# Kernel tuning notes

Hardware: AMD Instinct MI355X
Metric: run time of the kernel (lower is better)

The kernel has to match this reference:

```python
import jax, jax.numpy as jnp
import numpy as np

NUM_SPHERICAL = 7   # L
NUM_RADIAL = 6      # K
CUTOFF = 5.0
ENV_P = 6           # envelope exponent 5 -> p = exponent + 1
N_EDGES = 500000
N_PAIRS = 2000000


def _sph_jn_np(r, l):
    # spherical Bessel j_l via upward recurrence (numpy float64, host-side)
    j = np.sin(r) / r
    if l == 0:
        return j
    jp = np.sin(r) / r**2 - np.cos(r) / r
    for i in range(1, l):
        j, jp = jp, (2 * i + 1) / r * jp - j
    return jp


def _bessel_zeros(L, K):
    # zeros of j_0 are n*pi; zeros of j_l interlace zeros of j_{l-1} (bisection)
    prev = np.arange(1, K + L + 1, dtype=np.float64) * np.pi
    zeros = [prev[:K].copy()]
    for l in range(1, L):
        lo, hi = prev[:-1].copy(), prev[1:].copy()
        flo = _sph_jn_np(lo, l)
        for _ in range(100):
            mid = 0.5 * (lo + hi)
            fm = _sph_jn_np(mid, l)
            same = np.sign(fm) == np.sign(flo)
            lo = np.where(same, mid, lo)
            flo = np.where(same, fm, flo)
            hi = np.where(same, hi, mid)
        prev = 0.5 * (lo + hi)
        zeros.append(prev[:K].copy())
    return np.stack(zeros)  # (L, K)


_Z = _bessel_zeros(NUM_SPHERICAL, NUM_RADIAL)
_NORM = np.stack([1.0 / np.sqrt(0.5 * _sph_jn_np(_Z[l], l + 1) ** 2)
                  for l in range(NUM_SPHERICAL)])
Z = jnp.asarray(_Z, dtype=jnp.float32)        # (L, K) Bessel zeros z_{l,n}
NORM = jnp.asarray(_NORM, dtype=jnp.float32)  # (L, K) normalizers c_{l,n}
_SPH_C = jnp.asarray(np.sqrt((2 * np.arange(NUM_SPHERICAL) + 1) / (4 * np.pi)),
                     dtype=jnp.float32)       # Y_l^0 prefactors


def _sph_jn(t, l):
    # spherical Bessel j_l(t), upward recurrence (matches closed-form sympy basis)
    j = jnp.sin(t) / t
    if l == 0:
        return j
    jp = jnp.sin(t) / t**2 - jnp.cos(t) / t
    for i in range(1, l):
        j, jp = jp, (2 * i + 1) / t * jp - j
    return jp


def _envelope(x):
    # DimeNet polynomial envelope u(x) = 1/x + a x^{p-1} + b x^p + c x^{p+1}
    p = ENV_P
    a = -(p + 1) * (p + 2) / 2.0
    b = float(p * (p + 2))
    c = -p * (p + 1) / 2.0
    return 1.0 / x + a * x ** (p - 1) + b * x ** p + c * x ** (p + 1)


def setup_inputs() -> dict:
    key = jax.random.key(0)
    k1, k2, k3 = jax.random.split(key, 3)
    distances = jax.random.normal(k1, (N_EDGES, 3), dtype=jnp.float32) * 2.0
    senders = jax.random.randint(k2, (N_PAIRS,), 0, N_EDGES)
    receivers = jax.random.randint(k3, (N_PAIRS,), 0, N_EDGES)
    return {"distances": distances, "senders": senders, "receivers": receivers}


def reference(distances, senders, receivers):
    L, K = NUM_SPHERICAL, NUM_RADIAL
    dist = jnp.linalg.norm(distances, axis=-1, keepdims=True)     # (E, 1)
    normed_d = distances / dist                                   # (E, 3)
    x = dist / CUTOFF                                             # (E, 1)
    # radial Bessel basis: rbf[e, l, n] = c_{l,n} * j_l(z_{l,n} * x_e)
    rbf = jnp.stack([NORM[l] * _sph_jn(x * Z[l], l) for l in range(L)], axis=1)
    env = _envelope(x)                                            # (E, 1)
    rbf = rbf.reshape(-1, L * K) * env                            # (E, L*K)
    # angular basis: Y_l^0(theta) = sqrt((2l+1)/4pi) * P_l(cos theta)
    cos = jnp.einsum('pd,pd->p', normed_d[receivers], normed_d[senders])  # (P,)
    P_prev = jnp.ones_like(cos)
    P_cur = cos
    legs = [P_prev, P_cur]
    for l in range(1, L - 1):
        P_prev, P_cur = P_cur, ((2 * l + 1) * cos * P_cur - l * P_prev) / (l + 1)
        legs.append(P_cur)
    cbf = jnp.stack(legs[:L], axis=1) * _SPH_C                    # (P, L)
    # outer-product fuse: (P, L, K) -> (P, L*K)
    out = (rbf[senders].reshape(-1, L, K) * cbf[:, :, None]).reshape(-1, L * K)
    return out
```

## Files before the change

### kernel.cpp

```cpp
#include <hip/hip_runtime.h>
#include <math.h>

#define L_SPH 7
#define K_RAD 6
#define LK    42
#define TPB   256
#define PTPB  64
#define RSTR  48


typedef float f32x4 __attribute__((ext_vector_type(4)));
typedef float f32x2 __attribute__((ext_vector_type(2)));


struct SBConsts {
    float z[L_SPH][K_RAD];
    float nrm[L_SPH][K_RAD];
    float sphc[L_SPH];
};

static double host_sph_jn(double r, int l) {
    double j = sin(r) / r;
    if (l == 0) return j;
    double jp = sin(r) / (r * r) - cos(r) / r;
    for (int i = 1; i < l; i++) {
        double t = (2.0 * i + 1.0) / r * jp - j;
        j = jp; jp = t;
    }
    return jp;
}

static SBConsts make_consts() {
    const int L = L_SPH, K = K_RAD;
    double prev[L + K];
    for (int i = 0; i < L + K; i++) prev[i] = (i + 1) * M_PI;
    int plen = L + K;
    double zeros[L_SPH][K_RAD];
    for (int n = 0; n < K; n++) zeros[0][n] = prev[n];
    for (int l = 1; l < L; l++) {
        int m = plen - 1;
        double lo[L + K], hi[L + K], flo[L + K];
        for (int i = 0; i < m; i++) {
            lo[i] = prev[i]; hi[i] = prev[i + 1];
            flo[i] = host_sph_jn(lo[i], l);
        }
        for (int it = 0; it < 100; it++) {
            for (int i = 0; i < m; i++) {
                double mid = 0.5 * (lo[i] + hi[i]);
                double fm  = host_sph_jn(mid, l);
                bool same  = (fm >= 0.0) == (flo[i] >= 0.0);
                if (same) { lo[i] = mid; flo[i] = fm; }
                else      { hi[i] = mid; }
            }
        }
        for (int i = 0; i < m; i++) prev[i] = 0.5 * (lo[i] + hi[i]);
        plen = m;
        for (int n = 0; n < K; n++) zeros[l][n] = prev[n];
    }
    SBConsts c;
    for (int l = 0; l < L; l++) {
        for (int n = 0; n < K; n++) {
            c.z[l][n] = (float)zeros[l][n];
            double j1 = host_sph_jn(zeros[l][n], l + 1);
            c.nrm[l][n] = (float)(1.0 / sqrt(0.5 * j1 * j1));
        }
        c.sphc[l] = (float)sqrt((2.0 * l + 1.0) / (4.0 * M_PI));
    }
    return c;
}


__device__ __forceinline__ float sin_f32cr(float t) { return (float)sin((double)t); }
__device__ __forceinline__ void sincos_f32cr(float t, float& s, float& c) {
    double ds, dc;
    sincos((double)t, &ds, &dc);
    s = (float)ds; c = (float)dc;
}

__device__ void edge_row_f32(float dx, float dy, float dz, const SBConsts& c,
                             float* row, float& nx, float& ny, float& nz) {
#pragma clang fp contract(off)
    float s = dx * dx;
    s = s + dy * dy;
    s = s + dz * dz;
    float dist = (float)sqrt((double)s);
    nx = dx / dist; ny = dy / dist; nz = dz / dist;
    float x = dist / 5.0f;
    float x2 = x * x, x4 = x2 * x2;
    float x5 = x4 * x, x6 = x5 * x, x7 = x6 * x;
    float env = 1.0f / x;
    env = env + (-28.0f) * x5;
    env = env + 48.0f * x6;
    env = env + (-21.0f) * x7;
#pragma unroll
    for (int l = 0; l < L_SPH; l++) {
#pragma unroll
        for (int n = 0; n < K_RAD; n++) {
            float t  = x * c.z[l][n];
            float sn, co;
            if (l == 0) { sn = sin_f32cr(t); co = 0.0f; }
            else        { sincos_f32cr(t, sn, co); }
            float j  = sn / t;
            if (l > 0) {
                float t2 = t * t;
                float a1 = sn / t2;
                float a2 = co / t;
                float jp = a1 - a2;
#pragma unroll
                for (int i = 1; i < l; i++) {
                    float q  = (float)(2 * i + 1) / t;
                    float m  = q * jp;
                    float nj = m - j;
                    j = jp; jp = nj;
                }
                j = jp;
            }
            float rb = c.nrm[l][n] * j;
            row[l * K_RAD + n] = rb * env;
        }
    }
}

__device__ __forceinline__ void legendre_cbf(float cs, const float* sphc,
                                             float* cbf) {
#pragma clang fp contract(off)
    float P0 = 1.0f, P1 = cs;
    cbf[0] = sphc[0];
    cbf[1] = sphc[1] * cs;
#pragma unroll
    for (int l = 1; l < L_SPH - 1; l++) {
        float a  = (float)(2 * l + 1) * cs;
        float b  = a * P1;
        float d  = b - (float)l * P0;
        float Pn = d / (float)(l + 1);
        P0 = P1; P1 = Pn;
        cbf[l + 1] = sphc[l + 1] * Pn;
    }
}


__global__ __launch_bounds__(TPB) void edge_kernel(
        const float* __restrict__ d, float* __restrict__ rbf,
        float4* __restrict__ nd4, int nE, SBConsts c) {
    int e = blockIdx.x * TPB + threadIdx.x;
    if (e >= nE) return;
    float dx = d[3 * e], dy = d[3 * e + 1], dz = d[3 * e + 2];
    float row[LK], nx, ny, nz;
    edge_row_f32(dx, dy, dz, c, row, nx, ny, nz);
    nd4[e] = make_float4(nx, ny, nz, 0.0f);
    float4* o = (float4*)(rbf + (size_t)e * RSTR);
#pragma unroll
    for (int q = 0; q < 10; q++)
        o[q] = make_float4(row[4 * q], row[4 * q + 1], row[4 * q + 2], row[4 * q + 3]);
    o[10] = make_float4(row[40], row[41], nx, ny);
    o[11] = make_float4(nz, 0.0f, 0.0f, 0.0f);
}


__global__ __launch_bounds__(PTPB, 4) void pair_kernel(
        const int* __restrict__ snd, const int* __restrict__ rcv,
        const float* __restrict__ rbf, const float4* __restrict__ nd4,
        float* __restrict__ out, int nP, SBConsts c) {
#pragma clang fp contract(off)
    __shared__ float so[PTPB * LK];
    int p = blockIdx.x * PTPB + threadIdx.x;
    if (p < nP) {
        int s = snd[p], r = rcv[p];
        const float4* rowp = (const float4*)(rbf + (size_t)s * RSTR);
        float4 v[12];
#pragma unroll
        for (int q = 0; q < 12; q++) v[q] = rowp[q];
        float4 b = nd4[r];
        float ax = v[10].z, ay = v[10].w, az = v[11].x;
        float cs = ax * b.x;
        cs = cs + ay * b.y;
        cs = cs + az * b.z;
        float cbf[L_SPH];
        legendre_cbf(cs, c.sphc, cbf);
        float2* my = (float2*)&so[threadIdx.x * LK];
#pragma unroll
        for (int q = 0; q < 10; q++) {
            float4 vq = v[q];
            my[2 * q]     = make_float2(vq.x * cbf[(4 * q + 0) / K_RAD],
                                        vq.y * cbf[(4 * q + 1) / K_RAD]);
            my[2 * q + 1] = make_float2(vq.z * cbf[(4 * q + 2) / K_RAD],
                                        vq.w * cbf[(4 * q + 3) / K_RAD]);
        }
        my[20] = make_float2(v[10].x * cbf[6], v[10].y * cbf[6]);
    }
    __syncthreads();
    size_t base  = (size_t)blockIdx.x * (PTPB * LK);
    size_t limit = (size_t)nP * LK;
    if (base + PTPB * LK <= limit) {
        f32x4* o4 = (f32x4*)(out + base);
        const f32x4* s4 = (const f32x4*)so;
#pragma unroll
        for (int k = 0; k < 10; k++)
            __builtin_nontemporal_store(s4[threadIdx.x + k * PTPB],
                                        &o4[threadIdx.x + k * PTPB]);
        f32x2* o2 = (f32x2*)(out + base + 2560);
        const f32x2* s2 = (const f32x2*)(so + 2560);
        __builtin_nontemporal_store(s2[threadIdx.x], &o2[threadIdx.x]);
    } else {
        for (int k = 0; k < LK; k++) {
            size_t g = base + threadIdx.x + (size_t)k * PTPB;
            if (g < limit) out[g] = so[threadIdx.x + k * PTPB];
        }
    }
}


__global__ __launch_bounds__(TPB) void fused_kernel(
        const float* __restrict__ d, const int* __restrict__ snd,
        const int* __restrict__ rcv, float* __restrict__ out,
        int nP, SBConsts c) {
#pragma clang fp contract(off)
    int p = blockIdx.x * TPB + threadIdx.x;
    if (p >= nP) return;
    int s = snd[p], r = rcv[p];
    float row[LK], sx, sy, sz;
    edge_row_f32(d[3 * s], d[3 * s + 1], d[3 * s + 2], c, row, sx, sy, sz);
    float rx = d[3 * r], ry = d[3 * r + 1], rz = d[3 * r + 2];
    float t = rx * rx;  t = t + ry * ry;  t = t + rz * rz;
    float rd = (float)sqrt((double)t);
    float cs = sx * (rx / rd);
    cs = cs + sy * (ry / rd);
    cs = cs + sz * (rz / rd);
    float cbf[L_SPH];
    legendre_cbf(cs, c.sphc, cbf);
    float* o = out + (size_t)p * LK;
#pragma unroll
    for (int j = 0; j < LK; j++) o[j] = row[j] * cbf[j / K_RAD];
}


extern "C" void kernel_launch(void* const* d_in, const int* in_sizes, int n_in,
                              void* d_out, int out_size, void* d_ws, size_t ws_size,
                              hipStream_t stream) {
    static SBConsts c = make_consts();
    const float* dists = (const float*)d_in[0];
    const int*   snd   = (const int*)d_in[1];
    const int*   rcv   = (const int*)d_in[2];
    float*       out   = (float*)d_out;
    int nE = in_sizes[0] / 3;
    int nP = in_sizes[1];

    size_t rbf_bytes = (size_t)nE * RSTR * sizeof(float);
    size_t need = rbf_bytes + (size_t)nE * sizeof(float4);

    if (ws_size >= need) {
        float*  rbf = (float*)d_ws;
        float4* nd4 = (float4*)((char*)d_ws + rbf_bytes);
        edge_kernel<<<(nE + TPB - 1) / TPB, TPB, 0, stream>>>(dists, rbf, nd4, nE, c);
        pair_kernel<<<(nP + PTPB - 1) / PTPB, PTPB, 0, stream>>>(snd, rcv, rbf, nd4, out, nP, c);
    } else {
        fused_kernel<<<(nP + TPB - 1) / TPB, TPB, 0, stream>>>(dists, snd, rcv, out, nP, c);
    }
}
```

Baseline: 586.4 us.

## Split edge basis computation into per-element threads across edges and basis indices

New measurement: 591.0 us. About the same (+0.8%).

```diff
diff --git a/kernel.cpp b/kernel.cpp
--- a/kernel.cpp
+++ b/kernel.cpp
@@ -69,13 +69,159 @@
     return c;
 }
 
-
 __device__ __forceinline__ float sin_f32cr(float t) { return (float)sin((double)t); }
 __device__ __forceinline__ void sincos_f32cr(float t, float& s, float& c) {
     double ds, dc;
     sincos((double)t, &ds, &dc);
     s = (float)ds; c = (float)dc;
 }
+
+__device__ __forceinline__ void legendre_cbf(float cs, const float* sphc,
+                                             float* cbf) {
+#pragma clang fp contract(off)
+    float P0 = 1.0f, P1 = cs;
+    cbf[0] = sphc[0];
+    cbf[1] = sphc[1] * cs;
+#pragma unroll
+    for (int l = 1; l < L_SPH - 1; l++) {
+        float a  = (float)(2 * l + 1) * cs;
+        float b  = a * P1;
+        float d  = b - (float)l * P0;
+        float Pn = d / (float)(l + 1);
+        P0 = P1; P1 = Pn;
+        cbf[l + 1] = sphc[l + 1] * Pn;
+    }
+}
+
+
+__global__ __launch_bounds__(64) void init_tab(float* __restrict__ tab, SBConsts c) {
+    if (blockIdx.x != 0 || threadIdx.x != 0) return;
+#pragma unroll
+    for (int l = 0; l < L_SPH; l++)
+#pragma unroll
+        for (int n = 0; n < K_RAD; n++) {
+            tab[l * K_RAD + n]      = c.z[l][n];
+            tab[42 + l * K_RAD + n] = c.nrm[l][n];
+        }
+}
+
+
+__global__ __launch_bounds__(TPB) void edge_pre(
+        const float* __restrict__ d, float* __restrict__ rbf,
+        float4* __restrict__ nd4, int nE) {
+#pragma clang fp contract(off)
+    int e = blockIdx.x * TPB + threadIdx.x;
+    if (e >= nE) return;
+    float dx = d[3 * e], dy = d[3 * e + 1], dz = d[3 * e + 2];
+    float s = dx * dx;
+    s = s + dy * dy;
+    s = s + dz * dz;
+    float dist = (float)sqrt((double)s);
+    float nx = dx / dist, ny = dy / dist, nz = dz / dist;
+    float x = dist / 5.0f;
+    float x2 = x * x, x4 = x2 * x2;
+    float x5 = x4 * x, x6 = x5 * x, x7 = x6 * x;
+    float env = 1.0f / x;
+    env = env + (-28.0f) * x5;
+    env = env + 48.0f * x6;
+    env = env + (-21.0f) * x7;
+    nd4[e] = make_float4(nx, ny, nz, 0.0f);
+    float* row = rbf + (size_t)e * RSTR;
+    f32x2 xe; xe.x = x; xe.y = env;
+    *(f32x2*)(row + 42) = xe;
+    f32x4 dir; dir.x = nx; dir.y = ny; dir.z = nz; dir.w = 0.0f;
+    *(f32x4*)(row + 44) = dir;
+}
+
+
+__global__ __launch_bounds__(TPB, 4) void edge_basis(
+        const float* __restrict__ tab, float* __restrict__ rbf, int nE) {
+#pragma clang fp contract(off)
+    int i = blockIdx.x * TPB + threadIdx.x;
+    if (i >= nE * LK) return;
+    unsigned ui = (unsigned)i;
+    unsigned e = ui / (unsigned)LK;
+    int j = (int)(ui - e * (unsigned)LK);
+    const float* row = rbf + (size_t)e * RSTR;
+    f32x2 xe = *(const f32x2*)(row + 42);
+    float x = xe.x, env = xe.y;
+    float zj = tab[j], nrmj = tab[42 + j];
+    int l = j / K_RAD;
+    float t = x * zj;
+    float sn, co;
+    if (l == 0) { sn = sin_f32cr(t); co = 0.0f; }
+    else        { sincos_f32cr(t, sn, co); }
+    float jj = sn / t;
+    if (l > 0) {
+        float t2 = t * t;
+        float a1 = sn / t2;
+        float a2 = co / t;
+        float jp = a1 - a2;
+        for (int ii = 1; ii < l; ii++) {
+            float q  = (float)(2 * ii + 1) / t;
+            float m  = q * jp;
+            float nj = m - jj;
+            jj = jp; jp = nj;
+        }
+        jj = jp;
+    }
+    float rb = nrmj * jj;
+    rbf[(size_t)e * RSTR + j] = rb * env;
+}
+
+
+__global__ __launch_bounds__(PTPB, 4) void pair_kernel(
+        const int* __restrict__ snd, const int* __restrict__ rcv,
+        const float* __restrict__ rbf, const float4* __restrict__ nd4,
+        float* __restrict__ out, int nP, SBConsts c) {
+#pragma clang fp contract(off)
+    __shared__ float so[PTPB * LK];
+    int p = blockIdx.x * PTPB + threadIdx.x;
+    if (p < nP) {
+        int s = snd[p], r = rcv[p];
+        const float4* rowp = (const float4*)(rbf + (size_t)s * RSTR);
+        float4 v[12];
+#pragma unroll
+        for (int q = 0; q < 12; q++) v[q] = rowp[q];
+        float4 b = nd4[r];
+        float ax = v[11].x, ay = v[11].y, az = v[11].z;
+        float cs = ax * b.x;
+        cs = cs + ay * b.y;
+        cs = cs + az * b.z;
+        float cbf[L_SPH];
+        legendre_cbf(cs, c.sphc, cbf);
+        float2* my = (float2*)&so[threadIdx.x * LK];
+#pragma unroll
+        for (int q = 0; q < 10; q++) {
+            float4 vq = v[q];
+            my[2 * q]     = make_float2(vq.x * cbf[(4 * q + 0) / K_RAD],
+                                        vq.y * cbf[(4 * q + 1) / K_RAD]);
+            my[2 * q + 1] = make_float2(vq.z * cbf[(4 * q + 2) / K_RAD],
+                                        vq.w * cbf[(4 * q + 3) / K_RAD]);
+        }
+        my[20] = make_float2(v[10].x * cbf[6], v[10].y * cbf[6]);
+    }
+    __syncthreads();
+    size_t base  = (size_t)blockIdx.x * (PTPB * LK);
+    size_t limit = (size_t)nP * LK;
+    if (base + PTPB * LK <= limit) {
+        f32x4* o4 = (f32x4*)(out + base);
+        const f32x4* s4 = (const f32x4*)so;
+#pragma unroll
+        for (int k = 0; k < 10; k++)
+            __builtin_nontemporal_store(s4[threadIdx.x + k * PTPB],
+                                        &o4[threadIdx.x + k * PTPB]);
+        f32x2* o2 = (f32x2*)(out + base + 2560);
+        const f32x2* s2 = (const f32x2*)(so + 2560);
+        __builtin_nontemporal_store(s2[threadIdx.x], &o2[threadIdx.x]);
+    } else {
+        for (int k = 0; k < LK; k++) {
+            size_t g = base + threadIdx.x + (size_t)k * PTPB;
+            if (g < limit) out[g] = so[threadIdx.x + k * PTPB];
+        }
+    }
+}
+
 
 __device__ void edge_row_f32(float dx, float dy, float dz, const SBConsts& c,
                              float* row, float& nx, float& ny, float& nz) {
@@ -120,95 +266,6 @@
         }
     }
 }
-
-__device__ __forceinline__ void legendre_cbf(float cs, const float* sphc,
-                                             float* cbf) {
-#pragma clang fp contract(off)
-    float P0 = 1.0f, P1 = cs;
-    cbf[0] = sphc[0];
-    cbf[1] = sphc[1] * cs;
-#pragma unroll
-    for (int l = 1; l < L_SPH - 1; l++) {
-        float a  = (float)(2 * l + 1) * cs;
-        float b  = a * P1;
-        float d  = b - (float)l * P0;
-        float Pn = d / (float)(l + 1);
-        P0 = P1; P1 = Pn;
-        cbf[l + 1] = sphc[l + 1] * Pn;
-    }
-}
-
-
-__global__ __launch_bounds__(TPB) void edge_kernel(
-        const float* __restrict__ d, float* __restrict__ rbf,
-        float4* __restrict__ nd4, int nE, SBConsts c) {
-    int e = blockIdx.x * TPB + threadIdx.x;
-    if (e >= nE) return;
-    float dx = d[3 * e], dy = d[3 * e + 1], dz = d[3 * e + 2];
-    float row[LK], nx, ny, nz;
-    edge_row_f32(dx, dy, dz, c, row, nx, ny, nz);
-    nd4[e] = make_float4(nx, ny, nz, 0.0f);
-    float4* o = (float4*)(rbf + (size_t)e * RSTR);
-#pragma unroll
-    for (int q = 0; q < 10; q++)
-        o[q] = make_float4(row[4 * q], row[4 * q + 1], row[4 * q + 2], row[4 * q + 3]);
-    o[10] = make_float4(row[40], row[41], nx, ny);
-    o[11] = make_float4(nz, 0.0f, 0.0f, 0.0f);
-}
-
-
-__global__ __launch_bounds__(PTPB, 4) void pair_kernel(
-        const int* __restrict__ snd, const int* __restrict__ rcv,
-        const float* __restrict__ rbf, const float4* __restrict__ nd4,
-        float* __restrict__ out, int nP, SBConsts c) {
-#pragma clang fp contract(off)
-    __shared__ float so[PTPB * LK];
-    int p = blockIdx.x * PTPB + threadIdx.x;
-    if (p < nP) {
-        int s = snd[p], r = rcv[p];
-        const float4* rowp = (const float4*)(rbf + (size_t)s * RSTR);
-        float4 v[12];
-#pragma unroll
-        for (int q = 0; q < 12; q++) v[q] = rowp[q];
-        float4 b = nd4[r];
-        float ax = v[10].z, ay = v[10].w, az = v[11].x;
-        float cs = ax * b.x;
-        cs = cs + ay * b.y;
-        cs = cs + az * b.z;
-        float cbf[L_SPH];
-        legendre_cbf(cs, c.sphc, cbf);
-        float2* my = (float2*)&so[threadIdx.x * LK];
-#pragma unroll
-        for (int q = 0; q < 10; q++) {
-            float4 vq = v[q];
-            my[2 * q]     = make_float2(vq.x * cbf[(4 * q + 0) / K_RAD],
-                                        vq.y * cbf[(4 * q + 1) / K_RAD]);
-            my[2 * q + 1] = make_float2(vq.z * cbf[(4 * q + 2) / K_RAD],
-                                        vq.w * cbf[(4 * q + 3) / K_RAD]);
-        }
-        my[20] = make_float2(v[10].x * cbf[6], v[10].y * cbf[6]);
-    }
-    __syncthreads();
-    size_t base  = (size_t)blockIdx.x * (PTPB * LK);
-    size_t limit = (size_t)nP * LK;
-    if (base + PTPB * LK <= limit) {
-        f32x4* o4 = (f32x4*)(out + base);
-        const f32x4* s4 = (const f32x4*)so;
-#pragma unroll
-        for (int k = 0; k < 10; k++)
-            __builtin_nontemporal_store(s4[threadIdx.x + k * PTPB],
-                                        &o4[threadIdx.x + k * PTPB]);
-        f32x2* o2 = (f32x2*)(out + base + 2560);
-        const f32x2* s2 = (const f32x2*)(so + 2560);
-        __builtin_nontemporal_store(s2[threadIdx.x], &o2[threadIdx.x]);
-    } else {
-        for (int k = 0; k < LK; k++) {
-            size_t g = base + threadIdx.x + (size_t)k * PTPB;
-            if (g < limit) out[g] = so[threadIdx.x + k * PTPB];
-        }
-    }
-}
-
 
 __global__ __launch_bounds__(TPB) void fused_kernel(
         const float* __restrict__ d, const int* __restrict__ snd,
@@ -245,13 +302,19 @@
     int nE = in_sizes[0] / 3;
     int nP = in_sizes[1];
 
-    size_t rbf_bytes = (size_t)nE * RSTR * sizeof(float);
-    size_t need = rbf_bytes + (size_t)nE * sizeof(float4);
+    size_t rbf_b = (size_t)nE * RSTR * sizeof(float);
+    size_t nd4_b = (size_t)nE * sizeof(float4);
+    size_t tab_b = 512;
+    size_t need  = rbf_b + nd4_b + tab_b;
 
     if (ws_size >= need) {
         float*  rbf = (float*)d_ws;
-        float4* nd4 = (float4*)((char*)d_ws + rbf_bytes);
-        edge_kernel<<<(nE + TPB - 1) / TPB, TPB, 0, stream>>>(dists, rbf, nd4, nE, c);
+        float4* nd4 = (float4*)((char*)d_ws + rbf_b);
+        float*  tab = (float*)((char*)d_ws + rbf_b + nd4_b);
+        int nB = nE * LK;
+        init_tab  <<<1, 64, 0, stream>>>(tab, c);
+        edge_pre  <<<(nE + TPB - 1) / TPB, TPB, 0, stream>>>(dists, rbf, nd4, nE);
+        edge_basis<<<(nB + TPB - 1) / TPB, TPB, 0, stream>>>(tab, rbf, nE);
         pair_kernel<<<(nP + PTPB - 1) / PTPB, PTPB, 0, stream>>>(snd, rcv, rbf, nd4, out, nP, c);
     } else {
         fused_kernel<<<(nP + TPB - 1) / TPB, TPB, 0, stream>>>(dists, snd, rcv, out, nP, c);
```
